# Kernel optimization log

Measured on AMD Instinct MI355X. Metric: run time of the kernel, lower is better.

## Reference

```python
import jax, jax.numpy as jnp
import numpy as np

S, LC = 4096, 16
N_WORD, N_CHAR = 100000, 128
CHAR_DIM, CHAR_HIDDEN = 64, 128
N_DIM, N_HIDDEN, N_TAG = 256, 512, 64


def setup_inputs() -> dict:
    key = jax.random.key(0)
    ks = jax.random.split(key, 16)
    rn = lambda k, shape, s=0.1: (jax.random.normal(k, shape, jnp.float32) * s)
    inp = {
        'char_emb': rn(ks[0], (N_CHAR, CHAR_DIM), 1.0),
        'char_Wih': rn(ks[1], (4 * CHAR_HIDDEN, CHAR_DIM)),
        'char_Whh': rn(ks[2], (4 * CHAR_HIDDEN, CHAR_HIDDEN)),
        'char_bih': rn(ks[3], (4 * CHAR_HIDDEN,)),
        'char_bhh': rn(ks[4], (4 * CHAR_HIDDEN,)),
        'word_emb': rn(ks[5], (N_WORD, N_DIM), 1.0),
        'Wih': rn(ks[6], (4 * N_HIDDEN, N_DIM + CHAR_HIDDEN)),
        'Whh': rn(ks[7], (4 * N_HIDDEN, N_HIDDEN)),
        'bih': rn(ks[8], (4 * N_HIDDEN,)),
        'bhh': rn(ks[9], (4 * N_HIDDEN,)),
        'W1': rn(ks[10], (N_TAG, N_HIDDEN)),
        'b1': rn(ks[11], (N_TAG,)),
        'x': jax.random.randint(ks[12], (S,), 0, N_WORD),
        'chars': jax.random.randint(ks[13], (S, LC), 0, N_CHAR),
        'char_lens': jax.random.randint(ks[14], (S,), 1, LC + 1),
    }
    return inp


def _lstm(xs, mask, Wih, Whh, bih, bhh):
    # xs: [T, B, In], mask: [T, B] bool. PyTorch gate order: i, f, g, o.
    T, B, _ = xs.shape
    H = Whh.shape[1]
    def step(carry, inp):
        h, c = carry
        x_t, m_t = inp
        g = x_t @ Wih.T + bih + h @ Whh.T + bhh  # [B, 4H]
        i, f, gg, o = jnp.split(g, 4, axis=-1)
        c_new = jax.nn.sigmoid(f) * c + jax.nn.sigmoid(i) * jnp.tanh(gg)
        h_new = jax.nn.sigmoid(o) * jnp.tanh(c_new)
        m = m_t[:, None]
        h2 = jnp.where(m, h_new, h)
        c2 = jnp.where(m, c_new, c)
        return (h2, c2), h2
    init = (jnp.zeros((B, H), xs.dtype), jnp.zeros((B, H), xs.dtype))
    (h_fin, _), hs = jax.lax.scan(step, init, (xs, mask))
    return hs, h_fin


def reference(char_emb, char_Wih, char_Whh, char_bih, char_bhh,
              word_emb, Wih, Whh, bih, bhh, W1, b1,
              x, chars, char_lens):
    # --- char-level LSTM, all S words batched (replaces per-word Python loop) ---
    cx = char_emb[chars]                      # [S, LC, char_dim]
    cx = jnp.transpose(cx, (1, 0, 2))         # [LC, S, char_dim]
    cmask = jnp.arange(LC)[:, None] < char_lens[None, :]  # [LC, S]
    _, char_h = _lstm(cx, cmask, char_Wih, char_Whh, char_bih, char_bhh)  # [S, char_hidden]

    # --- word-level LSTM over the sentence (batch 1, as in original) ---
    wx = word_emb[x]                          # [S, n_dim]
    feat = jnp.concatenate([wx, char_h], axis=-1)[:, None, :]  # [S, 1, n_dim+char_hidden]
    wmask = jnp.ones((feat.shape[0], 1), bool)
    hs, _ = _lstm(feat, wmask, Wih, Whh, bih, bhh)  # [S, 1, n_hidden]
    hs = hs[:, 0, :]

    logits = hs @ W1.T + b1                   # [S, n_tag]
    return jax.nn.log_softmax(logits, axis=-1)
```

## Files before the change

kernel.cpp:

```cpp
#include <hip/hip_runtime.h>
#include <hip/hip_bf16.h>


#define OFF_FLAG  0
#define OFF_CEMB  16
#define OFF_CWIH  8208
#define OFF_CBIH  40976
#define OFF_CBHH  41488
#define OFF_CWHH  42000
#define OFF_BIH   107536
#define OFF_BHH   109584
#define OFF_W1T   111632
#define OFF_CGE   144400
#define OFF_CH    209936
#define OFF_XP2   734224
#define OFF_HH    4928528

#define SENT 0xFFFFFFFFu

__device__ __forceinline__ float sigf(float x) { return 1.0f / (1.0f + __expf(-x)); }
__device__ __forceinline__ float tanh_f(float x) { return 2.0f * sigf(2.0f * x) - 1.0f; }
__device__ __forceinline__ float b2f_lo(unsigned u) { return __uint_as_float(u << 16); }
__device__ __forceinline__ float b2f_hi(unsigned u) { return __uint_as_float(u & 0xFFFF0000u); }

__global__ void detect_kernel(const unsigned* __restrict__ w, int* __restrict__ flagp) {
    unsigned v = w[threadIdx.x];
    unsigned e = (v >> 7) & 0xFF;
    int inr = (e >= 100 && e <= 140) ? 1 : 0;
    unsigned long long m = __ballot(inr);
    if (threadIdx.x == 0) flagp[0] = (__popcll(m) >= 56) ? 1 : 0;
}

__global__ void convf_kernel(const void* __restrict__ s, float* __restrict__ d,
                             int n, const int* __restrict__ flagp) {
    int i = blockIdx.x * 256 + threadIdx.x;
    if (i >= n) return;
    d[i] = flagp[0] ? __bfloat162float(((const __hip_bfloat16*)s)[i])
                    : ((const float*)s)[i];
}

__global__ void w1t_kernel(const void* __restrict__ W1, float* __restrict__ W1T,
                           const int* __restrict__ flagp) {
    int i = blockIdx.x * 256 + threadIdx.x;
    int j = i & 63, k = i >> 6;
    W1T[i] = flagp[0] ? __bfloat162float(((const __hip_bfloat16*)W1)[j * 512 + k])
                      : ((const float*)W1)[j * 512 + k];
}

__global__ void __launch_bounds__(256) cge_kernel(
    const float* __restrict__ cemb, const float* __restrict__ cWih,
    const float* __restrict__ cbih, const float* __restrict__ cbhh,
    float* __restrict__ cge)
{
    __shared__ float xe[64];
    int c = blockIdx.x, tid = threadIdx.x;
    if (tid < 64) xe[tid] = cemb[c * 64 + tid];
    __syncthreads();
#pragma unroll
    for (int rep = 0; rep < 2; ++rep) {
        int j = rep * 256 + tid;
        float acc = cbih[j] + cbhh[j];
#pragma unroll 8
        for (int k = 0; k < 64; ++k)
            acc += xe[k] * cWih[j * 64 + k];
        cge[c * 512 + j] = acc;
    }
}

__global__ void __launch_bounds__(256) char_lstm_kernel(
    const float* __restrict__ cge, const float* __restrict__ Whh,
    const int* __restrict__ chars, const int* __restrict__ lens,
    float* __restrict__ char_h)
{
    __shared__ float hls[16][128];
    int tid = threadIdx.x;
    int wl = tid >> 4, sl = tid & 15;
    int w = blockIdx.x * 16 + wl;
    int len = lens[w];
    const int* cw = chars + w * 16;
    float c[8];
#pragma unroll
    for (int q = 0; q < 8; ++q) { c[q] = 0.0f; hls[wl][sl * 8 + q] = 0.0f; }

    for (int t = 0; t < 16; ++t) {
        __syncthreads();
        int ch = cw[t];
        const float* xg = cge + ch * 512;
        float acc[4][8];
#pragma unroll
        for (int g = 0; g < 4; ++g)
#pragma unroll
            for (int q = 0; q < 8; ++q)
                acc[g][q] = xg[g * 128 + sl * 8 + q];

        const float4* h4 = (const float4*)hls[wl];
#pragma unroll
        for (int g = 0; g < 4; ++g) {
            const float4* wbase = ((const float4*)Whh) + (g * 128 + sl * 8) * 32;
            for (int k4 = 0; k4 < 32; ++k4) {
                float4 hv = h4[k4];
#pragma unroll
                for (int q = 0; q < 8; ++q) {
                    float4 wv = wbase[q * 32 + k4];
                    acc[g][q] += wv.x * hv.x + wv.y * hv.y + wv.z * hv.z + wv.w * hv.w;
                }
            }
        }
        __syncthreads();
        if (t < len) {
#pragma unroll
            for (int q = 0; q < 8; ++q) {
                float iv = sigf(acc[0][q]);
                float fv = sigf(acc[1][q]);
                float gv = tanh_f(acc[2][q]);
                float ov = sigf(acc[3][q]);
                c[q] = fv * c[q] + iv * gv;
                hls[wl][sl * 8 + q] = ov * tanh_f(c[q]);
            }
        }
    }
    __syncthreads();
#pragma unroll
    for (int q = 0; q < 8; ++q)
        char_h[w * 128 + sl * 8 + q] = hls[wl][sl * 8 + q];
}

__global__ void __launch_bounds__(256) xp2_kernel(
    const void* __restrict__ wemb, const int* __restrict__ x,
    const float* __restrict__ char_h, const void* __restrict__ Wraw,
    const float* __restrict__ bih, const float* __restrict__ bhh,
    __hip_bfloat16* __restrict__ xp2, const int* __restrict__ flagp)
{
    __shared__ float feat[16][384];
    int flag = flagp[0];
    int tid = threadIdx.x, tl = tid >> 4, sl = tid & 15;
    int t = blockIdx.x * 16 + tl;
    int xw = x[t];
    for (int idx = sl; idx < 384; idx += 16) {
        float v;
        if (idx < 256)
            v = flag ? __bfloat162float(((const __hip_bfloat16*)wemb)[(size_t)xw * 256 + idx])
                     : ((const float*)wemb)[(size_t)xw * 256 + idx];
        else
            v = char_h[t * 128 + (idx - 256)];
        feat[tl][idx] = v;
    }
    __syncthreads();

    const float4* f4 = (const float4*)feat[tl];
    for (int rb = 0; rb < 4; ++rb) {
        int r0 = rb * 512 + sl * 32;
        for (int qc = 0; qc < 4; ++qc) {
            int rr = r0 + qc * 8;
            float acc[8];
#pragma unroll
            for (int q = 0; q < 8; ++q)
                acc[q] = bih[rr + q] + bhh[rr + q];
            if (!flag) {
                const float4* wb = ((const float4*)Wraw) + (size_t)rr * 96;
                for (int k4 = 0; k4 < 96; ++k4) {
                    float4 fv = f4[k4];
#pragma unroll
                    for (int q = 0; q < 8; ++q) {
                        float4 wv = wb[q * 96 + k4];
                        acc[q] += wv.x * fv.x + wv.y * fv.y + wv.z * fv.z + wv.w * fv.w;
                    }
                }
            } else {
                const uint2* wb = ((const uint2*)Wraw) + (size_t)rr * 96;
                for (int k4 = 0; k4 < 96; ++k4) {
                    float4 fv = f4[k4];
#pragma unroll
                    for (int q = 0; q < 8; ++q) {
                        uint2 wv = wb[q * 96 + k4];
                        acc[q] += b2f_lo(wv.x) * fv.x + b2f_hi(wv.x) * fv.y
                                + b2f_lo(wv.y) * fv.z + b2f_hi(wv.y) * fv.w;
                    }
                }
            }
#pragma unroll
            for (int q = 0; q < 8; ++q)
                xp2[(size_t)t * 2048 + rr + q] = __float2bfloat16(acc[q]);
        }
    }
}

__global__ void __launch_bounds__(1024, 4) word_lstm_kernel(
    const __hip_bfloat16* __restrict__ xp2, const void* __restrict__ Whh_raw,
    float* __restrict__ h_hist, const int* __restrict__ flagp)
{
    __shared__ float hbuf[16][576];
    __shared__ float hout[32];
    int flag = flagp[0];
    int wg = blockIdx.x;
    int tid = threadIdx.x;
    int wave = tid >> 6, lane = tid & 63;
    int sp = lane >> 5;
    int g  = (lane >> 3) & 3;
    int kk = lane & 7;
    int slot = wg * 32 + wave * 2 + sp;
    int grow = g * 512 + slot;

    float4 wreg[16];
    if (!flag) {
        const float4* wr = (const float4*)((const float*)Whh_raw + (size_t)grow * 512 + kk * 64);
#pragma unroll
        for (int i = 0; i < 16; ++i) wreg[i] = wr[i];
    } else {
        const uint2* wr = (const uint2*)((const unsigned short*)Whh_raw + (size_t)grow * 512 + kk * 64);
#pragma unroll
        for (int i = 0; i < 16; ++i) {
            uint2 u = wr[i];
            wreg[i] = make_float4(b2f_lo(u.x), b2f_hi(u.x), b2f_lo(u.y), b2f_hi(u.y));
        }
    }

    unsigned* hview = (unsigned*)h_hist;
    float* wbuf = hbuf[wave];
    float c = 0.0f;
    int dead = 0;

    for (int t = 0; t < 4096; ++t) {
        float xv = __bfloat162float(xp2[(size_t)t * 2048 + grow]);

        if (t == 0) {
#pragma unroll
            for (int i = 0; i < 8; ++i)
                wbuf[(2 * i + (lane >> 5)) * 36 + (lane & 31)] = 0.0f;
        } else {
            const unsigned* src = hview + (size_t)(t - 1) * 512 + lane;
            unsigned v[8];
            unsigned spins = 0;
            for (;;) {
#pragma unroll
                for (int i = 0; i < 8; ++i)
                    v[i] = __hip_atomic_load(src + (size_t)i * 64, __ATOMIC_RELAXED,
                                             __HIP_MEMORY_SCOPE_AGENT);
                int ok = 1;
#pragma unroll
                for (int i = 0; i < 8; ++i) ok &= (v[i] != SENT);
                if (dead || __all(ok)) break;
                if (++spins > (1u << 20)) { dead = 1; break; }
            }
            if (dead) {
#pragma unroll
                for (int i = 0; i < 8; ++i)
                    if (v[i] == SENT) v[i] = __float_as_uint(12345.0f);
            }
#pragma unroll
            for (int i = 0; i < 8; ++i)
                wbuf[(2 * i + (lane >> 5)) * 36 + (lane & 31)] = __uint_as_float(v[i]);
        }

        const float4* p0 = (const float4*)(wbuf + kk * 72);
        const float4* p1 = (const float4*)(wbuf + kk * 72 + 36);
        float acc = 0.0f;
#pragma unroll
        for (int i = 0; i < 8; ++i) {
            float4 hv = p0[i];
            acc += wreg[i].x * hv.x + wreg[i].y * hv.y +
                   wreg[i].z * hv.z + wreg[i].w * hv.w;
        }
#pragma unroll
        for (int i = 0; i < 8; ++i) {
            float4 hv = p1[i];
            acc += wreg[8 + i].x * hv.x + wreg[8 + i].y * hv.y +
                   wreg[8 + i].z * hv.z + wreg[8 + i].w * hv.w;
        }
        acc += __shfl_xor(acc, 1);
        acc += __shfl_xor(acc, 2);
        acc += __shfl_xor(acc, 4);
        float gvt = acc + xv;

        float iv = __shfl(gvt, sp * 32 + 0);
        float fv = __shfl(gvt, sp * 32 + 8);
        float gg = __shfl(gvt, sp * 32 + 16);
        float ov = __shfl(gvt, sp * 32 + 24);
        c = sigf(fv) * c + sigf(iv) * tanh_f(gg);
        float h = sigf(ov) * tanh_f(c);

        if ((lane & 31) == 0) hout[wave * 2 + sp] = h;
        __syncthreads();

        if (wave == 0 && lane < 32)
            __hip_atomic_store(hview + (size_t)t * 512 + wg * 32 + lane,
                               __float_as_uint(hout[lane]),
                               __ATOMIC_RELAXED, __HIP_MEMORY_SCOPE_AGENT);
    }
}

__global__ void __launch_bounds__(64) out_kernel(
    const float* __restrict__ h_hist, const float* __restrict__ W1T,
    const void* __restrict__ b1raw, void* __restrict__ out,
    const int* __restrict__ flagp)
{
    __shared__ float hb[512];
    int flag = flagp[0];
    int t = blockIdx.x, j = threadIdx.x;
    const float4* src = (const float4*)(h_hist + (size_t)t * 512);
    ((float4*)hb)[j * 2] = src[j * 2];
    ((float4*)hb)[j * 2 + 1] = src[j * 2 + 1];
    __syncthreads();

    float acc = flag ? __bfloat162float(((const __hip_bfloat16*)b1raw)[j])
                     : ((const float*)b1raw)[j];
#pragma unroll 8
    for (int k = 0; k < 512; ++k)
        acc += hb[k] * W1T[k * 64 + j];

    float m = acc;
#pragma unroll
    for (int o = 32; o; o >>= 1) m = fmaxf(m, __shfl_xor(m, o));
    float e = __expf(acc - m);
    float s = e;
#pragma unroll
    for (int o = 32; o; o >>= 1) s += __shfl_xor(s, o);
    float r = acc - m - __logf(s);
    if (flag) ((__hip_bfloat16*)out)[t * 64 + j] = __float2bfloat16(r);
    else      ((float*)out)[t * 64 + j] = r;
}

extern "C" void kernel_launch(void* const* d_in, const int* in_sizes, int n_in,
                              void* d_out, int out_size, void* d_ws, size_t ws_size,
                              hipStream_t stream)
{
    (void)in_sizes; (void)n_in; (void)out_size; (void)ws_size;
    const void* char_emb = d_in[0];
    const void* char_Wih = d_in[1];
    const void* char_Whh = d_in[2];
    const void* char_bih = d_in[3];
    const void* char_bhh = d_in[4];
    const void* word_emb = d_in[5];
    const void* Wih      = d_in[6];
    const void* Whh      = d_in[7];
    const void* bih      = d_in[8];
    const void* bhh      = d_in[9];
    const void* W1       = d_in[10];
    const void* b1       = d_in[11];
    const int* x     = (const int*)d_in[12];
    const int* chars = (const int*)d_in[13];
    const int* lens  = (const int*)d_in[14];

    float* ws    = (float*)d_ws;
    int*   flagp = (int*)(ws + OFF_FLAG);
    float* cembf = ws + OFF_CEMB;
    float* cWihf = ws + OFF_CWIH;
    float* cbihf = ws + OFF_CBIH;
    float* cbhhf = ws + OFF_CBHH;
    float* cWhhf = ws + OFF_CWHH;
    float* bihf  = ws + OFF_BIH;
    float* bhhf  = ws + OFF_BHH;
    float* W1T   = ws + OFF_W1T;
    float* cge   = ws + OFF_CGE;
    float* charh = ws + OFF_CH;
    __hip_bfloat16* xp2 = (__hip_bfloat16*)(ws + OFF_XP2);
    float* hh    = ws + OFF_HH;

    hipMemsetAsync(hh, 0xFF, (size_t)4096 * 512 * 4, stream);

    detect_kernel<<<1, 64, 0, stream>>>((const unsigned*)char_emb, flagp);

    convf_kernel<<<(8192 + 255) / 256, 256, 0, stream>>>(char_emb, cembf, 8192, flagp);
    convf_kernel<<<(32768 + 255) / 256, 256, 0, stream>>>(char_Wih, cWihf, 32768, flagp);
    convf_kernel<<<2, 256, 0, stream>>>(char_bih, cbihf, 512, flagp);
    convf_kernel<<<2, 256, 0, stream>>>(char_bhh, cbhhf, 512, flagp);
    convf_kernel<<<(65536 + 255) / 256, 256, 0, stream>>>(char_Whh, cWhhf, 65536, flagp);
    convf_kernel<<<8, 256, 0, stream>>>(bih, bihf, 2048, flagp);
    convf_kernel<<<8, 256, 0, stream>>>(bhh, bhhf, 2048, flagp);
    w1t_kernel<<<128, 256, 0, stream>>>(W1, W1T, flagp);

    cge_kernel<<<128, 256, 0, stream>>>(cembf, cWihf, cbihf, cbhhf, cge);
    char_lstm_kernel<<<256, 256, 0, stream>>>(cge, cWhhf, chars, lens, charh);
    xp2_kernel<<<256, 256, 0, stream>>>(word_emb, x, charh, Wih, bihf, bhhf, xp2, flagp);
    word_lstm_kernel<<<16, 1024, 0, stream>>>(xp2, Whh, hh, flagp);
    out_kernel<<<4096, 64, 0, stream>>>(hh, W1T, b1, d_out, flagp);
}
```

Before: 12.64 ms.

## Remove per-step block barrier in word LSTM; spread waves over more blocks

The word-level LSTM now runs as 64 blocks of 256 threads instead of 16 blocks of 1024. Each wave publishes its own hidden values straight to global memory, so the per-step __syncthreads and shared staging are gone. It also prefetches the next step's input projection, splits the dot product into four independent accumulators, and uses explicit named weight registers. The aims are to cut intra-block barrier latency on the serial critical path and to shorten FMA dependency chains. In exchange there are more blocks and more individual global stores to poll, and the spin timeout is raised.

```diff
diff --git a/kernel.cpp b/kernel.cpp
--- a/kernel.cpp
+++ b/kernel.cpp
@@ -22,6 +22,9 @@
 __device__ __forceinline__ float tanh_f(float x) { return 2.0f * sigf(2.0f * x) - 1.0f; }
 __device__ __forceinline__ float b2f_lo(unsigned u) { return __uint_as_float(u << 16); }
 __device__ __forceinline__ float b2f_hi(unsigned u) { return __uint_as_float(u & 0xFFFF0000u); }
+__device__ __forceinline__ float4 dec2(uint2 u) {
+    return make_float4(b2f_lo(u.x), b2f_hi(u.x), b2f_lo(u.y), b2f_hi(u.y));
+}
 
 __global__ void detect_kernel(const unsigned* __restrict__ w, int* __restrict__ flagp) {
     unsigned v = w[threadIdx.x];
@@ -185,43 +188,47 @@
     }
 }
 
-__global__ void __launch_bounds__(1024, 4) word_lstm_kernel(
+__global__ void __launch_bounds__(256, 1) word_lstm_kernel(
     const __hip_bfloat16* __restrict__ xp2, const void* __restrict__ Whh_raw,
     float* __restrict__ h_hist, const int* __restrict__ flagp)
 {
-    __shared__ float hbuf[16][576];
-    __shared__ float hout[32];
+    __shared__ float hbuf[4][576];
     int flag = flagp[0];
-    int wg = blockIdx.x;
     int tid = threadIdx.x;
     int wave = tid >> 6, lane = tid & 63;
+    int wgid = blockIdx.x * 4 + wave;
     int sp = lane >> 5;
     int g  = (lane >> 3) & 3;
     int kk = lane & 7;
-    int slot = wg * 32 + wave * 2 + sp;
+    int slot = wgid * 2 + sp;
     int grow = g * 512 + slot;
 
-    float4 wreg[16];
+    float4 w00, w01, w02, w03, w04, w05, w06, w07;
+    float4 w08, w09, w10, w11, w12, w13, w14, w15;
     if (!flag) {
         const float4* wr = (const float4*)((const float*)Whh_raw + (size_t)grow * 512 + kk * 64);
-#pragma unroll
-        for (int i = 0; i < 16; ++i) wreg[i] = wr[i];
+        w00 = wr[0];  w01 = wr[1];  w02 = wr[2];  w03 = wr[3];
+        w04 = wr[4];  w05 = wr[5];  w06 = wr[6];  w07 = wr[7];
+        w08 = wr[8];  w09 = wr[9];  w10 = wr[10]; w11 = wr[11];
+        w12 = wr[12]; w13 = wr[13]; w14 = wr[14]; w15 = wr[15];
     } else {
         const uint2* wr = (const uint2*)((const unsigned short*)Whh_raw + (size_t)grow * 512 + kk * 64);
-#pragma unroll
-        for (int i = 0; i < 16; ++i) {
-            uint2 u = wr[i];
-            wreg[i] = make_float4(b2f_lo(u.x), b2f_hi(u.x), b2f_lo(u.y), b2f_hi(u.y));
-        }
+        w00 = dec2(wr[0]);  w01 = dec2(wr[1]);  w02 = dec2(wr[2]);  w03 = dec2(wr[3]);
+        w04 = dec2(wr[4]);  w05 = dec2(wr[5]);  w06 = dec2(wr[6]);  w07 = dec2(wr[7]);
+        w08 = dec2(wr[8]);  w09 = dec2(wr[9]);  w10 = dec2(wr[10]); w11 = dec2(wr[11]);
+        w12 = dec2(wr[12]); w13 = dec2(wr[13]); w14 = dec2(wr[14]); w15 = dec2(wr[15]);
     }
 
     unsigned* hview = (unsigned*)h_hist;
+    const unsigned short* xpr = (const unsigned short*)xp2;
     float* wbuf = hbuf[wave];
     float c = 0.0f;
     int dead = 0;
 
+    unsigned short xraw = xpr[grow];
+
     for (int t = 0; t < 4096; ++t) {
-        float xv = __bfloat162float(xp2[(size_t)t * 2048 + grow]);
+        unsigned short xraw_nx = (t < 4095) ? xpr[(size_t)(t + 1) * 2048 + grow] : (unsigned short)0;
 
         if (t == 0) {
 #pragma unroll
@@ -240,7 +247,7 @@
 #pragma unroll
                 for (int i = 0; i < 8; ++i) ok &= (v[i] != SENT);
                 if (dead || __all(ok)) break;
-                if (++spins > (1u << 20)) { dead = 1; break; }
+                if (++spins > (1u << 22)) { dead = 1; break; }
             }
             if (dead) {
 #pragma unroll
@@ -254,23 +261,25 @@
 
         const float4* p0 = (const float4*)(wbuf + kk * 72);
         const float4* p1 = (const float4*)(wbuf + kk * 72 + 36);
-        float acc = 0.0f;
-#pragma unroll
-        for (int i = 0; i < 8; ++i) {
-            float4 hv = p0[i];
-            acc += wreg[i].x * hv.x + wreg[i].y * hv.y +
-                   wreg[i].z * hv.z + wreg[i].w * hv.w;
-        }
-#pragma unroll
-        for (int i = 0; i < 8; ++i) {
-            float4 hv = p1[i];
-            acc += wreg[8 + i].x * hv.x + wreg[8 + i].y * hv.y +
-                   wreg[8 + i].z * hv.z + wreg[8 + i].w * hv.w;
-        }
+        float a0 = 0.0f, a1 = 0.0f, a2 = 0.0f, a3 = 0.0f;
+        {
+            float4 hv;
+#define FMA4_(A, W, HV) A += (W).x*(HV).x + (W).y*(HV).y + (W).z*(HV).z + (W).w*(HV).w
+            hv = p0[0]; FMA4_(a0, w00, hv);  hv = p0[1]; FMA4_(a1, w01, hv);
+            hv = p0[2]; FMA4_(a2, w02, hv);  hv = p0[3]; FMA4_(a3, w03, hv);
+            hv = p0[4]; FMA4_(a0, w04, hv);  hv = p0[5]; FMA4_(a1, w05, hv);
+            hv = p0[6]; FMA4_(a2, w06, hv);  hv = p0[7]; FMA4_(a3, w07, hv);
+            hv = p1[0]; FMA4_(a0, w08, hv);  hv = p1[1]; FMA4_(a1, w09, hv);
+            hv = p1[2]; FMA4_(a2, w10, hv);  hv = p1[3]; FMA4_(a3, w11, hv);
+            hv = p1[4]; FMA4_(a0, w12, hv);  hv = p1[5]; FMA4_(a1, w13, hv);
+            hv = p1[6]; FMA4_(a2, w14, hv);  hv = p1[7]; FMA4_(a3, w15, hv);
+#undef FMA4_
+        }
+        float acc = (a0 + a1) + (a2 + a3);
         acc += __shfl_xor(acc, 1);
         acc += __shfl_xor(acc, 2);
         acc += __shfl_xor(acc, 4);
-        float gvt = acc + xv;
+        float gvt = acc + __bfloat162float(*(const __hip_bfloat16*)&xraw);
 
         float iv = __shfl(gvt, sp * 32 + 0);
         float fv = __shfl(gvt, sp * 32 + 8);
@@ -279,13 +288,12 @@
         c = sigf(fv) * c + sigf(iv) * tanh_f(gg);
         float h = sigf(ov) * tanh_f(c);
 
-        if ((lane & 31) == 0) hout[wave * 2 + sp] = h;
-        __syncthreads();
-
-        if (wave == 0 && lane < 32)
-            __hip_atomic_store(hview + (size_t)t * 512 + wg * 32 + lane,
-                               __float_as_uint(hout[lane]),
+        if ((lane & 31) == 0)
+            __hip_atomic_store(hview + (size_t)t * 512 + slot,
+                               __float_as_uint(h),
                                __ATOMIC_RELAXED, __HIP_MEMORY_SCOPE_AGENT);
+
+        xraw = xraw_nx;
     }
 }
 
@@ -372,6 +380,6 @@
     cge_kernel<<<128, 256, 0, stream>>>(cembf, cWihf, cbihf, cbhhf, cge);
     char_lstm_kernel<<<256, 256, 0, stream>>>(cge, cWhhf, chars, lens, charh);
     xp2_kernel<<<256, 256, 0, stream>>>(word_emb, x, charh, Wih, bihf, bhhf, xp2, flagp);
-    word_lstm_kernel<<<16, 1024, 0, stream>>>(xp2, Whh, hh, flagp);
+    word_lstm_kernel<<<64, 256, 0, stream>>>(xp2, Whh, hh, flagp);
     out_kernel<<<4096, 64, 0, stream>>>(hh, W1T, b1, d_out, flagp);
 }
```

New measurement: 14.65 ms. +15.9%, slower.
